# Kernel tuning notes

Measured on AMD Instinct MI355X. Metric: run time of the kernel, lower is better.

## Reference

```python
import jax, jax.numpy as jnp
import numpy as np

B, S, DIN, DQ, DK = 4, 2048, 1024, 64, 64
NEG_INF = -jnp.inf


def _make_mask(sq, sk):
    # Mirrors createMask: causal mask (-inf where key_idx > query_idx),
    # except 3 randomly chosen (row, col) 'global token' pairs left at 0.
    # torch version uses random.sample; we use a fixed numpy RNG for determinism.
    rng = np.random.default_rng(0)
    g_rows = rng.choice(sk, 3, replace=False)  # sampled from range(lrlen)
    g_cols = rng.choice(sq, 3, replace=False)  # sampled from range(sequence_len)
    row = jnp.arange(sq)[:, None]
    col = jnp.arange(sk)[None, :]
    mask = jnp.where(col > row, NEG_INF, 0.0).astype(jnp.float32)
    mask = mask.at[jnp.asarray(g_rows), jnp.asarray(g_cols)].set(0.0)
    return mask  # [sq, sk]


def setup_inputs() -> dict:
    key = jax.random.key(0)
    ks = jax.random.split(key, 9)
    sc = 1.0 / np.sqrt(DIN)
    return {
        "q": jax.random.normal(ks[0], (B, S, DIN), jnp.float32),
        "k": jax.random.normal(ks[1], (B, S, DIN), jnp.float32),
        "v": jax.random.normal(ks[2], (B, S, DIN), jnp.float32),
        "Wq": jax.random.normal(ks[3], (DIN, DQ), jnp.float32) * sc,
        "bq": jax.random.normal(ks[4], (DQ,), jnp.float32) * sc,
        "Wk": jax.random.normal(ks[5], (DIN, DK), jnp.float32) * sc,
        "bk": jax.random.normal(ks[6], (DK,), jnp.float32) * sc,
        "Wv": jax.random.normal(ks[7], (DIN, DK), jnp.float32) * sc,
        "bv": jax.random.normal(ks[8], (DK,), jnp.float32) * sc,
    }


def reference(q, k, v, Wq, bq, Wk, bk, Wv, bv):
    Q = q @ Wq + bq            # [B,S,DQ]
    K = k @ Wk + bk            # [B,S,DK]
    V = v @ Wv + bv            # [B,S,DK]
    scores = jnp.einsum("bqd,bkd->bqk", Q, K)  # [B,S,S]
    mask = _make_mask(scores.shape[-2], scores.shape[-1])
    denom = jnp.asarray(K.shape[-1], jnp.float32) ** 0.5
    # NOTE: original adds mask BEFORE dividing by sqrt(d_k); -inf survives division.
    attn = jax.nn.softmax((scores + mask) / denom, axis=-1)
    return jnp.einsum("bqk,bkd->bqd", attn, V)  # [B,S,DK]
```

## Files before the change

### kernel.cpp

```cpp
#include <hip/hip_runtime.h>
#include <cstdint>
#include <cstddef>
#include <math.h>

#define SEQ    2048
#define NBATCH 4
#define DIN    1024
#define DH     64

typedef __attribute__((ext_vector_type(8))) short  short8;
typedef __attribute__((ext_vector_type(4))) float  floatx4;

#define MFMA16(a, b, c) __builtin_amdgcn_mfma_f32_16x16x32_bf16((a), (b), (c), 0, 0, 0)

__device__ __forceinline__ unsigned short f2bf(float x) {
  unsigned u = __float_as_uint(x);
  return (unsigned short)((u + 0x8000u) >> 16);
}
__device__ __forceinline__ float bf2f(unsigned short h) {
  return __uint_as_float(((unsigned)h) << 16);
}

__device__ __forceinline__ void async_cp16(const void* g, void* l) {
  __builtin_amdgcn_global_load_lds(
      (const __attribute__((address_space(1))) void*)g,
      (__attribute__((address_space(3))) void*)l, 16, 0, 0);
}

template <int OFF>
__device__ __forceinline__ void gldw(short8 &d, unsigned long long a) {
  asm volatile("global_load_dwordx4 %0, %1, off offset:%2"
               : "=v"(d) : "v"(a), "n"(OFF));
}
#define WAITV(N) asm volatile("s_waitcnt vmcnt(" #N ")" ::: "memory")
#define SB()     __builtin_amdgcn_sched_barrier(0)
#define BAR()    __builtin_amdgcn_s_barrier()

#define DSR(dst, ra, OFF)                                                      \
  asm volatile("ds_read_b128 %0, %1 offset:%2" : "=v"(dst) : "v"(ra), "n"(OFF))

namespace nprng {

struct PCG64 {
  __uint128_t state, inc;
  bool has_uint32;
  uint32_t uinteger;
};

static inline void pcg_step(PCG64 &g) {
  const __uint128_t MULT =
      (((__uint128_t)0x2360ed051fc65da4ULL) << 64) | 0x4385df649fccf645ULL;
  g.state = g.state * MULT + g.inc;
}

static inline uint64_t pcg_output(const PCG64 &g) {
  uint64_t hi = (uint64_t)(g.state >> 64);
  uint64_t lo = (uint64_t)g.state;
  uint64_t x = hi ^ lo;
  unsigned rot = (unsigned)(g.state >> 122) & 63u;
  return (x >> rot) | (x << ((64u - rot) & 63u));
}

static inline uint64_t pcg_next64(PCG64 &g) { pcg_step(g); return pcg_output(g); }

static inline uint32_t pcg_next32(PCG64 &g) {
  if (g.has_uint32) { g.has_uint32 = false; return g.uinteger; }
  uint64_t n = pcg_next64(g);
  g.has_uint32 = true;
  g.uinteger = (uint32_t)(n >> 32);
  return (uint32_t)(n & 0xffffffffu);
}

static inline void pcg_seed_from_seedseq0(PCG64 &g) {
  const uint32_t MULT_A = 0x931e8875u;
  const uint32_t MULT_B = 0x58f38dedu;
  const uint32_t MIX_L  = 0xca01f9ddu;
  const uint32_t MIX_R  = 0x4973f715u;
  uint32_t hc = 0x43b0d7e5u;
  uint32_t pool[4];
  for (int i = 0; i < 4; i++) {
    uint32_t v = 0u;
    v ^= hc; hc *= MULT_A; v *= hc; v ^= v >> 16;
    pool[i] = v;
  }
  for (int is = 0; is < 4; is++) {
    for (int id = 0; id < 4; id++) {
      if (is == id) continue;
      uint32_t h = pool[is];
      h ^= hc; hc *= MULT_A; h *= hc; h ^= h >> 16;
      uint32_t r = (pool[id] * MIX_L) ^ (h * MIX_R);
      r ^= r >> 16;
      pool[id] = r;
    }
  }
  uint32_t hb = 0x8b51f9ddu;
  uint32_t w[8];
  for (int i = 0; i < 8; i++) {
    uint32_t v = pool[i & 3];
    v ^= hb; hb *= MULT_B; v *= hb; v ^= v >> 16;
    w[i] = v;
  }
  uint64_t sv[4];
  for (int k = 0; k < 4; k++)
    sv[k] = (uint64_t)w[2 * k] | ((uint64_t)w[2 * k + 1] << 32);
  __uint128_t initstate = (((__uint128_t)sv[0]) << 64) | sv[1];
  __uint128_t initseq   = (((__uint128_t)sv[2]) << 64) | sv[3];
  g.state = 0; g.inc = (initseq << 1) | 1;
  pcg_step(g);
  g.state += initstate;
  pcg_step(g);
  g.has_uint32 = false; g.uinteger = 0;
}

static inline uint32_t bounded32(PCG64 &g, uint32_t rng ) {
  if (rng == 0) return 0;
  const uint32_t rng_excl = rng + 1u;
  uint64_t m = (uint64_t)pcg_next32(g) * (uint64_t)rng_excl;
  uint32_t leftover = (uint32_t)m;
  if (leftover < rng_excl) {
    const uint32_t threshold = (uint32_t)(0xffffffffu - rng) % rng_excl;
    while (leftover < threshold) {
      m = (uint64_t)pcg_next32(g) * (uint64_t)rng_excl;
      leftover = (uint32_t)m;
    }
  }
  return (uint32_t)(m >> 32);
}

static inline void choice3_2048(PCG64 &g, long long idx[3]) {
  const int pop = 2048, sz = 3;
  uint64_t hs[4] = { (uint64_t)-1, (uint64_t)-1, (uint64_t)-1, (uint64_t)-1 };
  const uint64_t mask = 3;
  for (int j = pop - sz; j < pop; j++) {
    uint64_t val = (uint64_t)bounded32(g, (uint32_t)j);
    uint64_t loc = val & mask;
    while (hs[loc] != (uint64_t)-1 && hs[loc] != val) loc = (loc + 1) & mask;
    if (hs[loc] == (uint64_t)-1) {
      hs[loc] = val;
      idx[j - pop + sz] = (long long)val;
    } else {
      loc = (uint64_t)j & mask;
      while (hs[loc] != (uint64_t)-1) loc = (loc + 1) & mask;
      hs[loc] = (uint64_t)j;
      idx[j - pop + sz] = (long long)j;
    }
  }
  for (int i = 2; i >= 1; i--) {
    uint32_t j = bounded32(g, (uint32_t)i);
    long long t = idx[j]; idx[j] = idx[i]; idx[i] = t;
  }
}

}

__global__ __launch_bounds__(256) void wtrans_kernel(
    const float* __restrict__ Wq, const float* __restrict__ Wk,
    const float* __restrict__ Wv, unsigned short* __restrict__ WTc) {
  const int u = blockIdx.x * 256 + threadIdx.x;
  const int l   = u & 63;
  const int fi  = (u >> 6) & 7;
  const int nch = (u >> 9) & 1;
  const int kc  = (u >> 10) & 7;
  const int p   = u >> 13;
  const int f   = fi & 1;
  const int ks  = fi >> 1;
  const float* W = (p == 0) ? Wq : (p == 1) ? Wk : Wv;
  const int n  = nch * 32 + f * 16 + (l & 15);
  const int k0 = kc * 128 + ks * 32 + ((l >> 4) * 8);
  short8 v;
#pragma unroll
  for (int j = 0; j < 8; j++) v[j] = (short)f2bf(W[(size_t)(k0 + j) * 64 + n]);
  *((short8*)WTc + u) = v;
}

__global__ __launch_bounds__(256, 3) void proj_kernel(
    const float* __restrict__ xq, const float* __restrict__ xk,
    const float* __restrict__ xv, const unsigned short* __restrict__ WTc,
    const float* __restrict__ bq, const float* __restrict__ bk,
    const float* __restrict__ bv,
    unsigned short* __restrict__ Qf, unsigned short* __restrict__ Kf,
    unsigned short* __restrict__ Vf) {
  const int m0g  = blockIdx.x * 32;
  const int proj = m0g >> 13;
  const int m0   = m0g & 8191;
  const float* X    = (proj == 0) ? xq : (proj == 1) ? xk : xv;
  const float* bias = (proj == 0) ? bq : (proj == 1) ? bk : bv;

  const int tid  = threadIdx.x;
  const int w    = tid >> 6;
  const int l    = tid & 63;
  const int quad = l >> 4;
  const int lx   = l & 15;
  const int mr   = (w & 1) * 16;
  const int nc   = (w >> 1) * 32;

  __shared__ __align__(16) char LDSbuf[3 * 16384];

  const float* Xblk = X + (size_t)m0 * DIN;

  const char *ga0, *ga1, *ga2, *ga3;
  {
    const int lh = l >> 5, lu = l & 31;
#define GAX(i) ((const char*)(Xblk + (size_t)(8 * w + 2 * (i) + lh) * DIN) +    \
                (size_t)((lu ^ ((2 * (i) + lh) & 7)) << 4))
    ga0 = GAX(0); ga1 = GAX(1); ga2 = GAX(2); ga3 = GAX(3);
#undef GAX
  }

  const unsigned ldsb =
      (unsigned)(size_t)(__attribute__((address_space(3))) char*)LDSbuf;
  const unsigned ra0 = ldsb + (mr + lx) * 512 + (((quad * 2 + 0) ^ (lx & 7)) << 4);
  const unsigned ra1 = ldsb + (mr + lx) * 512 + (((quad * 2 + 1) ^ (lx & 7)) << 4);

  const unsigned long long wab =
      (unsigned long long)(const void*)((const short8*)WTc +
                                        ((size_t)(proj * 16 + (w >> 1))) * 512 + l);

  floatx4 acc0 = {0.f, 0.f, 0.f, 0.f}, acc1 = acc0;
  short8  wa[8], wb[8];
  floatx4 x0, x1, x2, x3, x4, x5, x6, x7;

#define STAGEX(KC, XB)                                                         \
  async_cp16(ga0 + (KC) * 512, LDSbuf + (XB) * 16384 + w * 4096 + 0);          \
  async_cp16(ga1 + (KC) * 512, LDSbuf + (XB) * 16384 + w * 4096 + 1024);       \
  async_cp16(ga2 + (KC) * 512, LDSbuf + (XB) * 16384 + w * 4096 + 2048);       \
  async_cp16(ga3 + (KC) * 512, LDSbuf + (XB) * 16384 + w * 4096 + 3072);

#define STAGEW(KC, WBUF)                                                       \
  { const unsigned long long p0 = wab + (KC) * 16384ull;                       \
    const unsigned long long p1 = p0 + 4096ull;                                \
    gldw<   0>(WBUF[0], p0); gldw<1024>(WBUF[1], p0);                          \
    gldw<2048>(WBUF[2], p0); gldw<3072>(WBUF[3], p0);                          \
    gldw<   0>(WBUF[4], p1); gldw<1024>(WBUF[5], p1);                          \
    gldw<2048>(WBUF[6], p1); gldw<3072>(WBUF[7], p1); }

#define READX(XB)                                                              \
  DSR(x0, ra0, (XB) * 16384 + 0);   DSR(x1, ra1, (XB) * 16384 + 0);            \
  DSR(x2, ra0, (XB) * 16384 + 128); DSR(x3, ra1, (XB) * 16384 + 128);          \
  DSR(x4, ra0, (XB) * 16384 + 256); DSR(x5, ra1, (XB) * 16384 + 256);          \
  DSR(x6, ra0, (XB) * 16384 + 384); DSR(x7, ra1, (XB) * 16384 + 384);          \
  asm volatile("s_waitcnt lgkmcnt(0)" ::: "memory");                           \
  __builtin_amdgcn_sched_barrier(0);

#define CVTM(f0, f1, w0, w1)                                                   \
  { short8 a_;                                                                 \
    a_[0] = f2bf(f0[0]); a_[1] = f2bf(f0[1]); a_[2] = f2bf(f0[2]); a_[3] = f2bf(f0[3]); \
    a_[4] = f2bf(f1[0]); a_[5] = f2bf(f1[1]); a_[6] = f2bf(f1[2]); a_[7] = f2bf(f1[3]); \
    acc0 = MFMA16(a_, w0, acc0); acc1 = MFMA16(a_, w1, acc1); }

#define DOMFMA(WBUF)                                                           \
  CVTM(x0, x1, WBUF[0], WBUF[1]); CVTM(x2, x3, WBUF[2], WBUF[3]);              \
  CVTM(x4, x5, WBUF[4], WBUF[5]); CVTM(x6, x7, WBUF[6], WBUF[7]);

  STAGEX(0, 0); STAGEW(0, wa); STAGEX(1, 1); STAGEW(1, wb); STAGEX(2, 2);

  WAITV(16); SB(); BAR(); READX(0); BAR(); DOMFMA(wa); STAGEW(2, wa); STAGEX(3, 0);
  WAITV(16); SB(); BAR(); READX(1); BAR(); DOMFMA(wb); STAGEW(3, wb); STAGEX(4, 1);
  WAITV(16); SB(); BAR(); READX(2); BAR(); DOMFMA(wa); STAGEW(4, wa); STAGEX(5, 2);
  WAITV(16); SB(); BAR(); READX(0); BAR(); DOMFMA(wb); STAGEW(5, wb); STAGEX(6, 0);
  WAITV(16); SB(); BAR(); READX(1); BAR(); DOMFMA(wa); STAGEW(6, wa); STAGEX(7, 1);
  WAITV(16); SB(); BAR(); READX(2); BAR(); DOMFMA(wb); STAGEW(7, wb);
  WAITV(12); SB(); BAR(); READX(0); BAR(); DOMFMA(wa);
  WAITV(0);  SB(); BAR(); READX(1); BAR(); DOMFMA(wb);

#undef STAGEX
#undef STAGEW
#undef READX
#undef CVTM
#undef DOMFMA

  float (*Cs)[68] = (float(*)[68])LDSbuf;
  const float bb0 = bias[nc + lx], bb1 = bias[nc + 16 + lx];
#pragma unroll
  for (int i = 0; i < 4; i++) {
    Cs[mr + quad * 4 + i][nc + lx]      = acc0[i] + bb0;
    Cs[mr + quad * 4 + i][nc + 16 + lx] = acc1[i] + bb1;
  }
  __syncthreads();

  const int bq_ = m0 >> 11;
  const int s0  = m0 & 2047;
  if (proj == 0) {
    const int ti = tid >> 7, s = (tid >> 6) & 1, ll = tid & 63;
    const int lxx = ll & 15, qq = ll >> 4;
    short8 v;
#pragma unroll
    for (int j = 0; j < 8; j++) v[j] = (short)f2bf(Cs[ti * 16 + lxx][s * 32 + qq * 8 + j]);
    char* dst = (char*)Qf + ((size_t)(bq_ * 128 + (s0 >> 4) + ti)) * 2048 + s * 1024 + ll * 16;
    *(short8*)dst = v;
  } else if (proj == 1) {
    const int ci = tid >> 7, s = (tid >> 6) & 1, ll = tid & 63;
    const int lxx = ll & 15, qq = ll >> 4;
    const int c = ((s0 >> 4) & 3) + ci;
    short8 v;
#pragma unroll
    for (int j = 0; j < 8; j++) v[j] = (short)f2bf(Cs[ci * 16 + lxx][s * 32 + qq * 8 + j]);
    char* dst = (char*)Kf + ((size_t)(bq_ * 32 + (s0 >> 6))) * 8192 + (c * 2 + s) * 1024 + ll * 16;
    *(short8*)dst = v;
  } else {
    const int c = tid >> 6, ll = tid & 63;
    const int lxx = ll & 15, qq = ll >> 4;
    const int sh = (s0 >> 5) & 1;
    short8 v;
#pragma unroll
    for (int j = 0; j < 8; j++) v[j] = (short)f2bf(Cs[qq * 8 + j][c * 16 + lxx]);
    char* dst = (char*)Vf + ((size_t)(bq_ * 32 + (s0 >> 6))) * 8192 + (sh * 4 + c) * 1024 + ll * 16;
    *(short8*)dst = v;
  }
}

__global__ __launch_bounds__(256, 2) void attn_kernel(
    const unsigned short* __restrict__ Qf, const unsigned short* __restrict__ Kf,
    const unsigned short* __restrict__ Vf, float* __restrict__ out,
    int R0, int C0, int R1, int C1, int R2, int C2) {
  const int b    = blockIdx.y;
  const int bx   = blockIdx.x;
  const int qi   = (bx & 1) ? (127 - (bx >> 1)) : (bx >> 1);
  const int q0   = qi * 16;
  const int tid  = threadIdx.x;
  const int w    = tid >> 6;
  const int l    = tid & 63;
  const int quad = l >> 4;
  const int lx   = l & 15;

  __shared__ unsigned short Ps[4][16][72];
  __shared__ float Os[4][16][64];
  __shared__ float mS[4][16], lS[4][16];
  __shared__ float lgS[3];
  __shared__ int   lgF[3];

  const char* Qc = (const char*)Qf + ((size_t)(b * 128 + qi)) * 2048 + l * 16;
  const short8 aq0 = *(const short8*)Qc;
  const short8 aq1 = *(const short8*)(Qc + 1024);

  floatx4 O[4];
  float m_i[4], l_i[4];
#pragma unroll
  for (int c = 0; c < 4; c++) O[c] = (floatx4){0.f, 0.f, 0.f, 0.f};
#pragma unroll
  for (int i = 0; i < 4; i++) { m_i[i] = -INFINITY; l_i[i] = 0.f; }

  const int T = (q0 + 79) >> 6;

  for (int t = w; t < T; t += 4) {
    const int k0 = t << 6;
    const bool mT = (t == T - 1);

    const char* Kc = (const char*)Kf + ((size_t)(b * 32 + t)) * 8192 + l * 16;
    const char* Vc = (const char*)Vf + ((size_t)(b * 32 + t)) * 8192 + l * 16;
    short8 kf[8], vf[8];
#pragma unroll
    for (int f = 0; f < 8; f++) {
      kf[f] = *(const short8*)(Kc + f * 1024);
      vf[f] = *(const short8*)(Vc + f * 1024);
    }

    floatx4 sc[4];
    __builtin_amdgcn_s_setprio(1);
#pragma unroll
    for (int c = 0; c < 4; c++) {
      sc[c] = (floatx4){0.f, 0.f, 0.f, 0.f};
      sc[c] = MFMA16(aq0, kf[2 * c], sc[c]);
      sc[c] = MFMA16(aq1, kf[2 * c + 1], sc[c]);
    }
    __builtin_amdgcn_s_setprio(0);

    float mt[4], al[4];
#pragma unroll
    for (int i = 0; i < 4; i++) {
      const int rowg = q0 + quad * 4 + i;
      float vmax = -INFINITY;
#pragma unroll
      for (int c = 0; c < 4; c++) {
        float v = sc[c][i] * 0.125f;
        if (mT && (k0 + 16 * c + lx) > rowg) v = -INFINITY;
        sc[c][i] = v;
        vmax = fmaxf(vmax, v);
      }
      mt[i] = vmax;
    }
#pragma unroll
    for (int i = 0; i < 4; i++) {
#pragma unroll
      for (int off = 8; off >= 1; off >>= 1)
        mt[i] = fmaxf(mt[i], __shfl_xor(mt[i], off));
      const float mn = fmaxf(m_i[i], mt[i]);
      al[i] = __expf(m_i[i] - mn);
      m_i[i] = mn;
      float s = 0.f;
#pragma unroll
      for (int c = 0; c < 4; c++) {
        float p = __expf(sc[c][i] - mn);
        Ps[w][quad * 4 + i][16 * c + lx] = f2bf(p);
        s += p;
      }
#pragma unroll
      for (int off = 8; off >= 1; off >>= 1) s += __shfl_xor(s, off);
      l_i[i] = l_i[i] * al[i] + s;
    }
#pragma unroll
    for (int c = 0; c < 4; c++)
#pragma unroll
      for (int i = 0; i < 4; i++) O[c][i] *= al[i];
    asm volatile("" ::: "memory");
    const short8 pf0 = *(const short8*)&Ps[w][lx][quad * 8];
    const short8 pf1 = *(const short8*)&Ps[w][lx][32 + quad * 8];
    __builtin_amdgcn_s_setprio(1);
#pragma unroll
    for (int c = 0; c < 4; c++) {
      O[c] = MFMA16(pf0, vf[c],     O[c]);
      O[c] = MFMA16(pf1, vf[4 + c], O[c]);
    }
    __builtin_amdgcn_s_setprio(0);
  }

  if (lx == 0) {
#pragma unroll
    for (int i = 0; i < 4; i++) {
      mS[w][quad * 4 + i] = m_i[i];
      lS[w][quad * 4 + i] = l_i[i];
    }
  }
#pragma unroll
  for (int c = 0; c < 4; c++)
#pragma unroll
    for (int i = 0; i < 4; i++) Os[w][quad * 4 + i][16 * c + lx] = O[c][i];

  if (w == 0) {
#pragma unroll
    for (int p = 0; p < 3; p++) {
      const int R = (p == 0) ? R0 : (p == 1) ? R1 : R2;
      const int C = (p == 0) ? C0 : (p == 1) ? C1 : C2;
      const int act = (R >= q0 && R < q0 + 16 && C > R);
      float d = 0.f;
      if (act) {
        const int dd = l;
        const char* qa = (const char*)Qf + ((size_t)(b * 128 + (R >> 4))) * 2048 +
                         (dd >> 5) * 1024 + ((R & 15) + ((dd >> 3) & 3) * 16) * 16 + (dd & 7) * 2;
        const char* ka = (const char*)Kf + ((size_t)(b * 32 + (C >> 6))) * 8192 +
                         (((C >> 4) & 3) * 2 + (dd >> 5)) * 1024 +
                         ((C & 15) + ((dd >> 3) & 3) * 16) * 16 + (dd & 7) * 2;
        d = bf2f(*(const unsigned short*)qa) * bf2f(*(const unsigned short*)ka);
#pragma unroll
        for (int off = 32; off >= 1; off >>= 1) d += __shfl_xor(d, off);
        d *= 0.125f;
      }
      if (l == 0) { lgF[p] = act; lgS[p] = d; }
    }
  }
  __syncthreads();

  {
    const int row = tid >> 4;
    const int d0  = (tid & 15) * 4;
    const int Rs[3] = {R0, R1, R2};
    const int Cs3[3] = {C0, C1, C2};

    float mf = -INFINITY;
#pragma unroll
    for (int w4 = 0; w4 < 4; w4++) mf = fmaxf(mf, mS[w4][row]);
#pragma unroll
    for (int p = 0; p < 3; p++)
      if (lgF[p] && (Rs[p] - q0) == row) mf = fmaxf(mf, lgS[p]);

    float lf = 0.f;
    float o0 = 0.f, o1 = 0.f, o2 = 0.f, o3 = 0.f;
#pragma unroll
    for (int w4 = 0; w4 < 4; w4++) {
      const float a = __expf(mS[w4][row] - mf);
      lf += a * lS[w4][row];
      const float* op = &Os[w4][row][d0];
      o0 += a * op[0]; o1 += a * op[1]; o2 += a * op[2]; o3 += a * op[3];
    }
#pragma unroll
    for (int p = 0; p < 3; p++) {
      if (lgF[p] && (Rs[p] - q0) == row) {
        const float pe = __expf(lgS[p] - mf);
        lf += pe;
        const int C = Cs3[p];
        float vv[4];
#pragma unroll
        for (int j = 0; j < 4; j++) {
          const int dim = d0 + j;
          const char* va = (const char*)Vf + ((size_t)(b * 32 + (C >> 6))) * 8192 +
                           (((C >> 5) & 1) * 4 + (dim >> 4)) * 1024 +
                           ((dim & 15) + ((C >> 3) & 3) * 16) * 16 + (C & 7) * 2;
          vv[j] = bf2f(*(const unsigned short*)va);
        }
        o0 += pe * vv[0]; o1 += pe * vv[1]; o2 += pe * vv[2]; o3 += pe * vv[3];
      }
    }
    const float inv = 1.0f / lf;
    float4 r;
    r.x = o0 * inv; r.y = o1 * inv; r.z = o2 * inv; r.w = o3 * inv;
    *(float4*)(out + ((size_t)b * SEQ + q0 + row) * 64 + d0) = r;
  }
}

extern "C" void kernel_launch(void* const* d_in, const int* in_sizes, int n_in,
                              void* d_out, int out_size, void* d_ws,
                              size_t ws_size, hipStream_t stream) {
  const float* xq = (const float*)d_in[0];
  const float* xk = (const float*)d_in[1];
  const float* xv = (const float*)d_in[2];
  const float* Wq = (const float*)d_in[3];
  const float* bq = (const float*)d_in[4];
  const float* Wk = (const float*)d_in[5];
  const float* bk = (const float*)d_in[6];
  const float* Wv = (const float*)d_in[7];
  const float* bv = (const float*)d_in[8];
  float* out = (float*)d_out;

  unsigned short* Qf  = (unsigned short*)d_ws;
  unsigned short* Kf  = Qf + (size_t)NBATCH * SEQ * 64;
  unsigned short* Vf  = Kf + (size_t)NBATCH * SEQ * 64;
  unsigned short* WTc = Vf + (size_t)NBATCH * SEQ * 64;

  nprng::PCG64 g;
  nprng::pcg_seed_from_seedseq0(g);
  long long rows[3], cols[3];
  nprng::choice3_2048(g, rows);
  nprng::choice3_2048(g, cols);

  wtrans_kernel<<<96, 256, 0, stream>>>(Wq, Wk, Wv, WTc);

  proj_kernel<<<768, 256, 0, stream>>>(xq, xk, xv, WTc, bq, bk, bv, Qf, Kf, Vf);

  dim3 agrid(SEQ / 16, NBATCH);
  attn_kernel<<<agrid, 256, 0, stream>>>(
      Qf, Kf, Vf, out, (int)rows[0], (int)cols[0], (int)rows[1], (int)cols[1],
      (int)rows[2], (int)cols[2]);
}
```

Before: 153.0 us.

## Convert projection inputs to bf16 in registers before staging to LDS

The projection kernel now loads fp32 X tiles into registers with global loads instead of async global-to-LDS copies. It converts them to packed bf16 once and writes them to a swizzled LDS buffer, so per-wave conversion work after the LDS read is removed and LDS usage drops from 48KB to 16KB. The pipeline becomes double-buffered with explicit register prefetch and extra barriers. Bias loads are hoisted to the start of the kernel. This trades async copy overlap for higher register pressure and extra VALU and LDS write traffic per tile.

```diff
diff --git a/kernel.cpp b/kernel.cpp
--- a/kernel.cpp
+++ b/kernel.cpp
@@ -10,6 +10,7 @@
 
 typedef __attribute__((ext_vector_type(8))) short  short8;
 typedef __attribute__((ext_vector_type(4))) float  floatx4;
+typedef __attribute__((ext_vector_type(2))) unsigned uint2v;
 
 #define MFMA16(a, b, c) __builtin_amdgcn_mfma_f32_16x16x32_bf16((a), (b), (c), 0, 0, 0)
 
@@ -20,24 +21,31 @@
 __device__ __forceinline__ float bf2f(unsigned short h) {
   return __uint_as_float(((unsigned)h) << 16);
 }
-
-__device__ __forceinline__ void async_cp16(const void* g, void* l) {
-  __builtin_amdgcn_global_load_lds(
-      (const __attribute__((address_space(1))) void*)g,
-      (__attribute__((address_space(3))) void*)l, 16, 0, 0);
-}
-
+__device__ __forceinline__ unsigned pk2(float a, float b) {
+  return (unsigned)f2bf(a) | ((unsigned)f2bf(b) << 16);
+}
+
+template <int OFF>
+__device__ __forceinline__ void gldx(floatx4 &d, unsigned long long a) {
+  asm volatile("global_load_dwordx4 %0, %1, off offset:%2"
+               : "=v"(d) : "v"(a), "n"(OFF));
+}
 template <int OFF>
 __device__ __forceinline__ void gldw(short8 &d, unsigned long long a) {
   asm volatile("global_load_dwordx4 %0, %1, off offset:%2"
                : "=v"(d) : "v"(a), "n"(OFF));
 }
+__device__ __forceinline__ void gldf(float &d, unsigned long long a) {
+  asm volatile("global_load_dword %0, %1, off" : "=v"(d) : "v"(a));
+}
 #define WAITV(N) asm volatile("s_waitcnt vmcnt(" #N ")" ::: "memory")
+#define WAITL()  asm volatile("s_waitcnt lgkmcnt(0)" ::: "memory")
 #define SB()     __builtin_amdgcn_sched_barrier(0)
 #define BAR()    __builtin_amdgcn_s_barrier()
-
 #define DSR(dst, ra, OFF)                                                      \
   asm volatile("ds_read_b128 %0, %1 offset:%2" : "=v"(dst) : "v"(ra), "n"(OFF))
+#define DSW(addr, val, OFF)                                                    \
+  asm volatile("ds_write_b64 %0, %1 offset:%2" :: "v"(addr), "v"(val), "n"(OFF) : "memory")
 
 namespace nprng {
 
@@ -194,23 +202,31 @@
   const int mr   = (w & 1) * 16;
   const int nc   = (w >> 1) * 32;
 
-  __shared__ __align__(16) char LDSbuf[3 * 16384];
-
-  const float* Xblk = X + (size_t)m0 * DIN;
-
-  const char *ga0, *ga1, *ga2, *ga3;
-  {
-    const int lh = l >> 5, lu = l & 31;
-#define GAX(i) ((const char*)(Xblk + (size_t)(8 * w + 2 * (i) + lh) * DIN) +    \
-                (size_t)((lu ^ ((2 * (i) + lh) & 7)) << 4))
-    ga0 = GAX(0); ga1 = GAX(1); ga2 = GAX(2); ga3 = GAX(3);
-#undef GAX
-  }
+  __shared__ __align__(16) char LDSbuf[2 * 8192];
+
+  float bb0, bb1;
+  gldf(bb0, (unsigned long long)(const void*)(bias + nc + lx));
+  gldf(bb1, (unsigned long long)(const void*)(bias + nc + 16 + lx));
+
+  const int srow = 8 * w + (l >> 3);
+  const unsigned long long xab = (unsigned long long)(const void*)
+      ((const char*)(X + (size_t)(m0 + srow) * DIN) + (l & 7) * 16);
 
   const unsigned ldsb =
       (unsigned)(size_t)(__attribute__((address_space(3))) char*)LDSbuf;
-  const unsigned ra0 = ldsb + (mr + lx) * 512 + (((quad * 2 + 0) ^ (lx & 7)) << 4);
-  const unsigned ra1 = ldsb + (mr + lx) * 512 + (((quad * 2 + 1) ^ (lx & 7)) << 4);
+  const int s7 = srow & 7;
+  const int u0 = (l >> 1) & 3;
+  const unsigned wbase = ldsb + srow * 256 + (l & 1) * 8;
+  const unsigned wr0 = wbase + (unsigned)(((0 << 2) | u0) ^ s7) * 16;
+  const unsigned wr1 = wbase + (unsigned)(((1 << 2) | u0) ^ s7) * 16;
+  const unsigned wr2 = wbase + (unsigned)(((2 << 2) | u0) ^ s7) * 16;
+  const unsigned wr3 = wbase + (unsigned)(((3 << 2) | u0) ^ s7) * 16;
+
+  const unsigned rbase = ldsb + (mr + lx) * 256;
+  const unsigned rd0 = rbase + (unsigned)(((0 << 2) | quad) ^ (lx & 7)) * 16;
+  const unsigned rd1 = rbase + (unsigned)(((1 << 2) | quad) ^ (lx & 7)) * 16;
+  const unsigned rd2 = rbase + (unsigned)(((2 << 2) | quad) ^ (lx & 7)) * 16;
+  const unsigned rd3 = rbase + (unsigned)(((3 << 2) | quad) ^ (lx & 7)) * 16;
 
   const unsigned long long wab =
       (unsigned long long)(const void*)((const short8*)WTc +
@@ -218,15 +234,13 @@
 
   floatx4 acc0 = {0.f, 0.f, 0.f, 0.f}, acc1 = acc0;
   short8  wa[8], wb[8];
-  floatx4 x0, x1, x2, x3, x4, x5, x6, x7;
-
-#define STAGEX(KC, XB)                                                         \
-  async_cp16(ga0 + (KC) * 512, LDSbuf + (XB) * 16384 + w * 4096 + 0);          \
-  async_cp16(ga1 + (KC) * 512, LDSbuf + (XB) * 16384 + w * 4096 + 1024);       \
-  async_cp16(ga2 + (KC) * 512, LDSbuf + (XB) * 16384 + w * 4096 + 2048);       \
-  async_cp16(ga3 + (KC) * 512, LDSbuf + (XB) * 16384 + w * 4096 + 3072);
-
-#define STAGEW(KC, WBUF)                                                       \
+  floatx4 ra0, ra1, ra2, ra3, rb0, rb1, rb2, rb3;
+
+#define LX(KC, R0, R1, R2, R3)                                                 \
+  gldx<(KC)*512 +   0>(R0, xab); gldx<(KC)*512 + 128>(R1, xab);                \
+  gldx<(KC)*512 + 256>(R2, xab); gldx<(KC)*512 + 384>(R3, xab);
+
+#define LW(KC, WBUF)                                                           \
   { const unsigned long long p0 = wab + (KC) * 16384ull;                       \
     const unsigned long long p1 = p0 + 4096ull;                                \
     gldw<   0>(WBUF[0], p0); gldw<1024>(WBUF[1], p0);                          \
@@ -234,43 +248,65 @@
     gldw<   0>(WBUF[4], p1); gldw<1024>(WBUF[5], p1);                          \
     gldw<2048>(WBUF[6], p1); gldw<3072>(WBUF[7], p1); }
 
-#define READX(XB)                                                              \
-  DSR(x0, ra0, (XB) * 16384 + 0);   DSR(x1, ra1, (XB) * 16384 + 0);            \
-  DSR(x2, ra0, (XB) * 16384 + 128); DSR(x3, ra1, (XB) * 16384 + 128);          \
-  DSR(x4, ra0, (XB) * 16384 + 256); DSR(x5, ra1, (XB) * 16384 + 256);          \
-  DSR(x6, ra0, (XB) * 16384 + 384); DSR(x7, ra1, (XB) * 16384 + 384);          \
-  asm volatile("s_waitcnt lgkmcnt(0)" ::: "memory");                           \
-  __builtin_amdgcn_sched_barrier(0);
-
-#define CVTM(f0, f1, w0, w1)                                                   \
-  { short8 a_;                                                                 \
-    a_[0] = f2bf(f0[0]); a_[1] = f2bf(f0[1]); a_[2] = f2bf(f0[2]); a_[3] = f2bf(f0[3]); \
-    a_[4] = f2bf(f1[0]); a_[5] = f2bf(f1[1]); a_[6] = f2bf(f1[2]); a_[7] = f2bf(f1[3]); \
-    acc0 = MFMA16(a_, w0, acc0); acc1 = MFMA16(a_, w1, acc1); }
-
-#define DOMFMA(WBUF)                                                           \
-  CVTM(x0, x1, WBUF[0], WBUF[1]); CVTM(x2, x3, WBUF[2], WBUF[3]);              \
-  CVTM(x4, x5, WBUF[4], WBUF[5]); CVTM(x6, x7, WBUF[6], WBUF[7]);
-
-  STAGEX(0, 0); STAGEW(0, wa); STAGEX(1, 1); STAGEW(1, wb); STAGEX(2, 2);
-
-  WAITV(16); SB(); BAR(); READX(0); BAR(); DOMFMA(wa); STAGEW(2, wa); STAGEX(3, 0);
-  WAITV(16); SB(); BAR(); READX(1); BAR(); DOMFMA(wb); STAGEW(3, wb); STAGEX(4, 1);
-  WAITV(16); SB(); BAR(); READX(2); BAR(); DOMFMA(wa); STAGEW(4, wa); STAGEX(5, 2);
-  WAITV(16); SB(); BAR(); READX(0); BAR(); DOMFMA(wb); STAGEW(5, wb); STAGEX(6, 0);
-  WAITV(16); SB(); BAR(); READX(1); BAR(); DOMFMA(wa); STAGEW(6, wa); STAGEX(7, 1);
-  WAITV(16); SB(); BAR(); READX(2); BAR(); DOMFMA(wb); STAGEW(7, wb);
-  WAITV(12); SB(); BAR(); READX(0); BAR(); DOMFMA(wa);
-  WAITV(0);  SB(); BAR(); READX(1); BAR(); DOMFMA(wb);
-
-#undef STAGEX
-#undef STAGEW
-#undef READX
-#undef CVTM
-#undef DOMFMA
+#define CW(R0, R1, R2, R3, BOFF)                                               \
+  { uint2v p0_, p1_, p2_, p3_;                                                 \
+    p0_[0] = pk2(R0[0], R0[1]); p0_[1] = pk2(R0[2], R0[3]);                    \
+    p1_[0] = pk2(R1[0], R1[1]); p1_[1] = pk2(R1[2], R1[3]);                    \
+    p2_[0] = pk2(R2[0], R2[1]); p2_[1] = pk2(R2[2], R2[3]);                    \
+    p3_[0] = pk2(R3[0], R3[1]); p3_[1] = pk2(R3[2], R3[3]);                    \
+    DSW(wr0, p0_, BOFF); DSW(wr1, p1_, BOFF);                                  \
+    DSW(wr2, p2_, BOFF); DSW(wr3, p3_, BOFF); }
+
+#define CONSUME(BOFF, WBUF)                                                    \
+  { floatx4 a0_, a1_, a2_, a3_;                                                \
+    DSR(a0_, rd0, BOFF); DSR(a1_, rd1, BOFF);                                  \
+    DSR(a2_, rd2, BOFF); DSR(a3_, rd3, BOFF);                                  \
+    WAITL(); SB();                                                             \
+    acc0 = MFMA16(*(short8*)&a0_, WBUF[0], acc0);                              \
+    acc1 = MFMA16(*(short8*)&a0_, WBUF[1], acc1);                              \
+    acc0 = MFMA16(*(short8*)&a1_, WBUF[2], acc0);                              \
+    acc1 = MFMA16(*(short8*)&a1_, WBUF[3], acc1);                              \
+    acc0 = MFMA16(*(short8*)&a2_, WBUF[4], acc0);                              \
+    acc1 = MFMA16(*(short8*)&a2_, WBUF[5], acc1);                              \
+    acc0 = MFMA16(*(short8*)&a3_, WBUF[6], acc0);                              \
+    acc1 = MFMA16(*(short8*)&a3_, WBUF[7], acc1); }
+
+  LX(0, ra0, ra1, ra2, ra3); LW(0, wa);
+  LX(1, rb0, rb1, rb2, rb3); LW(1, wb);
+
+  WAITV(12); SB();
+  CW(ra0, ra1, ra2, ra3, 0);    LX(2, ra0, ra1, ra2, ra3);
+  WAITL(); BAR(); CONSUME(0, wa);    LW(2, wa); BAR();
+  WAITV(12); SB();
+  CW(rb0, rb1, rb2, rb3, 8192); LX(3, rb0, rb1, rb2, rb3);
+  WAITL(); BAR(); CONSUME(8192, wb); LW(3, wb); BAR();
+  WAITV(12); SB();
+  CW(ra0, ra1, ra2, ra3, 0);    LX(4, ra0, ra1, ra2, ra3);
+  WAITL(); BAR(); CONSUME(0, wa);    LW(4, wa); BAR();
+  WAITV(12); SB();
+  CW(rb0, rb1, rb2, rb3, 8192); LX(5, rb0, rb1, rb2, rb3);
+  WAITL(); BAR(); CONSUME(8192, wb); LW(5, wb); BAR();
+  WAITV(12); SB();
+  CW(ra0, ra1, ra2, ra3, 0);    LX(6, ra0, ra1, ra2, ra3);
+  WAITL(); BAR(); CONSUME(0, wa);    LW(6, wa); BAR();
+  WAITV(12); SB();
+  CW(rb0, rb1, rb2, rb3, 8192); LX(7, rb0, rb1, rb2, rb3);
+  WAITL(); BAR(); CONSUME(8192, wb); LW(7, wb); BAR();
+  WAITV(12); SB();
+  CW(ra0, ra1, ra2, ra3, 0);
+  WAITL(); BAR(); CONSUME(0, wa); BAR();
+  WAITV(0); SB();
+  CW(rb0, rb1, rb2, rb3, 8192);
+  WAITL(); BAR(); CONSUME(8192, wb);
+
+#undef LX
+#undef LW
+#undef CW
+#undef CONSUME
+
+  __syncthreads();
 
   float (*Cs)[68] = (float(*)[68])LDSbuf;
-  const float bb0 = bias[nc + lx], bb1 = bias[nc + 16 + lx];
 #pragma unroll
   for (int i = 0; i < 4; i++) {
     Cs[mr + quad * 4 + i][nc + lx]      = acc0[i] + bb0;
```

After: 152.1 us (median of 2 runs). No clear change (-0.6%).
